# Performance work log

Hardware: AMD Instinct MI355X
Metric: run time of the kernel (lower is better)

## Reference

```python
import jax, jax.numpy as jnp
import numpy as np

NUM_HEADS = 16

def setup_inputs() -> dict:
    key = jax.random.key(0)
    ks = jax.random.split(key, 6)
    B, S, D = 2, 2048, 1024
    x = jax.random.normal(ks[0], (B, S, D), dtype=jnp.float32)
    s = 1.0 / np.sqrt(D)
    Wq = jax.random.normal(ks[1], (D, D), dtype=jnp.float32) * s
    Wk = jax.random.normal(ks[2], (D, D), dtype=jnp.float32) * s
    Wv = jax.random.normal(ks[3], (D, D), dtype=jnp.float32) * s
    Wff = jax.random.normal(ks[4], (D, D), dtype=jnp.float32) * s
    bff = jax.random.normal(ks[5], (D,), dtype=jnp.float32) * 0.01
    return {"x": x, "Wq": Wq, "Wk": Wk, "Wv": Wv, "Wff": Wff, "bff": bff}

def reference(x, Wq, Wk, Wv, Wff, bff):
    B, S, D = x.shape
    H = NUM_HEADS
    Dh = D // H
    # Q/K/V projections (bias-free Linears). Original scales Q by 1/sqrt(hidden_size).
    q = (x @ Wq.T) * (1.0 / jnp.sqrt(jnp.asarray(D, x.dtype)))
    k = x @ Wk.T
    v = x @ Wv.T
    q = q.reshape(B, S, H, Dh)
    k = k.reshape(B, S, H, Dh)
    v = v.reshape(B, S, H, Dh)
    # Blockwise online-softmax attention is mathematically identical to
    # full softmax attention over all keys (no causal mask in source).
    scores = jnp.einsum('bqhd,bkhd->bhqk', q, k)
    attn = jax.nn.softmax(scores, axis=-1)
    out = jnp.einsum('bhqk,bkhd->bqhd', attn, v).reshape(B, S, D)
    # Final feedforward Linear(hidden, hidden) with bias.
    return out @ Wff.T + bff
```

## Files before the change

kernel.cpp:

```cpp
#include <hip/hip_runtime.h>
#include <stdint.h>

typedef __attribute__((ext_vector_type(8))) short bf16x8;
typedef __attribute__((ext_vector_type(4))) float f32x4;

__device__ __forceinline__ uint16_t f2bf(float f) {
  union { float f; uint32_t u; } a; a.f = f;
  uint32_t u = a.u;
  u += 0x7FFFu + ((u >> 16) & 1u);
  return (uint16_t)(u >> 16);
}

__device__ __forceinline__ uint32_t pk_bf16(float a, float b) {
#if __has_builtin(__builtin_amdgcn_cvt_pk_bf16_f32)
  auto r = __builtin_amdgcn_cvt_pk_bf16_f32(a, b);
  uint32_t u; __builtin_memcpy(&u, &r, sizeof(u));
  return u;
#else
  return (uint32_t)f2bf(a) | ((uint32_t)f2bf(b) << 16);
#endif
}

__device__ __forceinline__ uint32_t pk_bf16_fast(float a, float b) {
#if __has_builtin(__builtin_amdgcn_cvt_pk_bf16_f32)
  auto r = __builtin_amdgcn_cvt_pk_bf16_f32(a, b);
  uint32_t u; __builtin_memcpy(&u, &r, sizeof(u));
  return u;
#else
  uint32_t ua, ub;
  __builtin_memcpy(&ua, &a, 4); __builtin_memcpy(&ub, &b, 4);
  return __builtin_amdgcn_perm(ub, ua, 0x07060302u);
#endif
}

__device__ __forceinline__ float fast_exp2(float x) {
#if __has_builtin(__builtin_amdgcn_exp2f)
  return __builtin_amdgcn_exp2f(x);
#else
  return exp2f(x);
#endif
}

__device__ __forceinline__ void gld_lds16(const uint16_t* g, uint16_t* l) {
  __builtin_amdgcn_global_load_lds(
      (const __attribute__((address_space(1))) void*)g,
      (__attribute__((address_space(3))) void*)l, 16, 0, 0);
}

__global__ void cast_all(const float* __restrict__ x, const float* __restrict__ wq,
                         const float* __restrict__ wk, const float* __restrict__ wv,
                         const float* __restrict__ wff,
                         uint16_t* __restrict__ xb, uint16_t* __restrict__ wqb,
                         uint16_t* __restrict__ wkb, uint16_t* __restrict__ wvb,
                         uint16_t* __restrict__ wffb) {
  int i = blockIdx.x * blockDim.x + threadIdx.x;
  const float* src; uint16_t* dst; int off;
  if (i < 1048576)      { src = x;   dst = xb;   off = i; }
  else if (i < 1310720) { src = wq;  dst = wqb;  off = i - 1048576; }
  else if (i < 1572864) { src = wk;  dst = wkb;  off = i - 1310720; }
  else if (i < 1835008) { src = wv;  dst = wvb;  off = i - 1572864; }
  else                  { src = wff; dst = wffb; off = i - 1835008; }
  float4 v = ((const float4*)src)[off];
  uint2 o; o.x = pk_bf16(v.x, v.y); o.y = pk_bf16(v.z, v.w);
  ((uint2*)dst)[off] = o;
}

__device__ __forceinline__ void gemm_tile(const uint16_t* __restrict__ Abase,
                                          const uint16_t* __restrict__ Bbase,
                                          uint16_t* lds, f32x4 acc[4][4]) {
  const int tid  = threadIdx.x;
  const int w    = tid >> 6;
  const int lane = tid & 63;
  const int wm   = w >> 1, wn = w & 1;
  const int lrow = lane & 15;
  const int quad = lane >> 4;
  const int srow = lane >> 3;
  const int lc   = (lane & 7) ^ srow;
  const int sx   = lrow & 7;
  uint16_t* a_lds = lds;
  uint16_t* b_lds = lds + 8192;

#pragma unroll
  for (int mt = 0; mt < 4; ++mt)
#pragma unroll
    for (int nt = 0; nt < 4; ++nt)
      acc[mt][nt] = (f32x4){0.f, 0.f, 0.f, 0.f};

  const uint16_t* ag = Abase + (size_t)(w * 32 + srow) * 1024 + lc * 8;
  const uint16_t* bg = Bbase + (size_t)(w * 32 + srow) * 1024 + lc * 8;

  for (int k0 = 0; k0 < 1024; k0 += 64) {
#pragma unroll
    for (int i8 = 0; i8 < 4; ++i8) {
      gld_lds16(ag + (size_t)i8 * 8 * 1024 + k0, a_lds + (w * 4 + i8) * 512);
      gld_lds16(bg + (size_t)i8 * 8 * 1024 + k0, b_lds + (w * 4 + i8) * 512);
    }
    __syncthreads();
#pragma unroll
    for (int ks = 0; ks < 2; ++ks) {
      bf16x8 af[4], bfr[4];
      const int c = ((ks * 4 + quad) ^ sx) << 3;
#pragma unroll
      for (int mt = 0; mt < 4; ++mt)
        af[mt] = *(const bf16x8*)(a_lds + (wm * 64 + mt * 16 + lrow) * 64 + c);
#pragma unroll
      for (int nt = 0; nt < 4; ++nt)
        bfr[nt] = *(const bf16x8*)(b_lds + (wn * 64 + nt * 16 + lrow) * 64 + c);
#pragma unroll
      for (int mt = 0; mt < 4; ++mt)
#pragma unroll
        for (int nt = 0; nt < 4; ++nt)
          acc[mt][nt] = __builtin_amdgcn_mfma_f32_16x16x32_bf16(af[mt], bfr[nt], acc[mt][nt], 0, 0, 0);
    }
    __syncthreads();
  }
}

__global__ __launch_bounds__(256) void gemm_qkv(
    const uint16_t* __restrict__ x,
    const uint16_t* __restrict__ wq, const uint16_t* __restrict__ wk, const uint16_t* __restrict__ wv,
    uint16_t* __restrict__ qo, uint16_t* __restrict__ ko, uint16_t* __restrict__ vto) {
  __shared__ __align__(16) uint16_t lds[17408];
  const int m0 = blockIdx.x * 128, n0 = blockIdx.y * 128, z = blockIdx.z;
  f32x4 acc[4][4];
  if (z < 2) {
    const uint16_t* W = (z == 0) ? wq : wk;
    gemm_tile(W + (size_t)n0 * 1024, x + (size_t)m0 * 1024, lds, acc);
  } else {
    gemm_tile(x + (size_t)m0 * 1024, wv + (size_t)n0 * 1024, lds, acc);
  }

  const int tid = threadIdx.x;
  const int lane = tid & 63, w = tid >> 6;
  const int wm = w >> 1, wn = w & 1, lrow = lane & 15, quad = lane >> 4;
  const float scale = (z == 0) ? 0.045084222f : 1.0f;

#pragma unroll
  for (int mt = 0; mt < 4; ++mt)
#pragma unroll
    for (int nt = 0; nt < 4; ++nt) {
      int i0 = wm * 64 + mt * 16 + quad * 4;
      int j  = wn * 64 + nt * 16 + lrow;
      uint2 dd;
      dd.x = pk_bf16(acc[mt][nt][0] * scale, acc[mt][nt][1] * scale);
      dd.y = pk_bf16(acc[mt][nt][2] * scale, acc[mt][nt][3] * scale);
      *(uint2*)(&lds[j * 136 + i0]) = dd;
    }
  __syncthreads();

  uint16_t* outp = (z == 0) ? qo : (z == 1) ? ko : vto;
  if (z < 2) {
#pragma unroll
    for (int it = 0; it < 8; ++it) {
      int idx = it * 256 + tid;
      int jj = idx >> 4, cc = idx & 15;
      uint4 v = *(const uint4*)(&lds[jj * 136 + cc * 8]);
      int m = m0 + jj, n = n0 + cc * 8;
      int b = m >> 11, s = m & 2047, h = n >> 6, dh = n & 63;
      *(uint4*)(outp + ((size_t)((b * 16 + h) * 2048 + s)) * 64 + dh) = v;
    }
  } else {
    int b = m0 >> 11, sbase = m0 & 2047;
#pragma unroll
    for (int it = 0; it < 8; ++it) {
      int idx = it * 256 + tid;
      int ff = idx >> 4, cc = idx & 15;
      uint4 v = *(const uint4*)(&lds[ff * 136 + cc * 8]);
      int n = n0 + ff, h = n >> 6, dh = n & 63;
      *(uint4*)(outp + ((size_t)((b * 16 + h) * 64 + dh)) * 2048 + sbase + cc * 8) = v;
    }
  }
}

__global__ __launch_bounds__(256) void gemm_ff(
    const uint16_t* __restrict__ ao, const uint16_t* __restrict__ wff,
    const float* __restrict__ bff, float* __restrict__ out) {
  __shared__ __align__(16) uint16_t lds[17408];
  const int m0 = blockIdx.x * 128, n0 = blockIdx.y * 128;
  f32x4 acc[4][4];
  gemm_tile(wff + (size_t)n0 * 1024, ao + (size_t)m0 * 1024, lds, acc);

  const int tid = threadIdx.x;
  const int lane = tid & 63, w = tid >> 6;
  const int wm = w >> 1, wn = w & 1, lrow = lane & 15, quad = lane >> 4;
  float* fl = (float*)lds;

#pragma unroll
  for (int p = 0; p < 2; ++p) {
    if (wm == p) {
#pragma unroll
      for (int mt = 0; mt < 4; ++mt)
#pragma unroll
        for (int nt = 0; nt < 4; ++nt) {
          int i0 = mt * 16 + quad * 4;
          int j  = wn * 64 + nt * 16 + lrow;
          *(f32x4*)(&fl[j * 68 + i0]) = acc[mt][nt];
        }
    }
    __syncthreads();
#pragma unroll
    for (int it = 0; it < 8; ++it) {
      int idx = it * 256 + tid;
      int jj = idx >> 4, cc = idx & 15;
      f32x4 v = *(const f32x4*)(&fl[jj * 68 + cc * 4]);
      int n = n0 + p * 64 + cc * 4;
      f32x4 bias = *(const f32x4*)(bff + n);
      f32x4 vv = v + bias;
      *(f32x4*)(out + (size_t)(m0 + jj) * 1024 + n) = vv;
    }
    __syncthreads();
  }
}

__global__ __launch_bounds__(256, 2) void attn(
    const uint16_t* __restrict__ q, const uint16_t* __restrict__ k,
    const uint16_t* __restrict__ vt, uint16_t* __restrict__ ao) {
  __shared__ __align__(16) uint16_t k_lds[2][4096];
  __shared__ __align__(16) uint16_t v_lds[2][4096];
  __shared__ __align__(16) uint16_t p_lds[2][8192];
  const int tid = threadIdx.x, w = tid >> 6, lane = tid & 63;
  const int lrow = lane & 15, quad = lane >> 4;
  const int srow = lane >> 3, lc = (lane & 7) ^ srow, sx = lrow & 7;
  const int pk = w >> 1, pq = w & 1;
  const int pswz = (lrow & 3) << 2;
  const int bh = blockIdx.y, qb = blockIdx.x;
  const uint16_t* Q = q  + (size_t)bh * (2048 * 64);
  const uint16_t* K = k  + (size_t)bh * (2048 * 64);
  const uint16_t* V = vt + (size_t)bh * (64 * 2048);

  const int qr0 = qb * 128;
  bf16x8 qf[8][2];
#pragma unroll
  for (int qh = 0; qh < 8; ++qh)
#pragma unroll
    for (int ks = 0; ks < 2; ++ks)
      qf[qh][ks] = *(const bf16x8*)(Q + (size_t)(qr0 + qh * 16 + lrow) * 64 + ks * 32 + quad * 8);

  f32x4 o[4][4];
#pragma unroll
  for (int qh = 0; qh < 4; ++qh)
#pragma unroll
    for (int dt = 0; dt < 4; ++dt) o[qh][dt] = (f32x4){0.f, 0.f, 0.f, 0.f};
  float ls[8] = {0.f, 0.f, 0.f, 0.f, 0.f, 0.f, 0.f, 0.f};
  bf16x8 vfr[4];

  auto stage = [&](int kb, int bi) {
#pragma unroll
    for (int i2 = 0; i2 < 2; ++i2) {
      int i8 = w * 2 + i2;
      gld_lds16(K + (size_t)(kb * 64 + i8 * 8 + srow) * 64 + lc * 8, &k_lds[bi][i8 * 512]);
      gld_lds16(V + (size_t)(i8 * 8 + srow) * 2048 + kb * 64 + lc * 8, &v_lds[bi][i8 * 512]);
    }
  };
  stage(0, 0);

  for (int kb = 0; kb < 32; ++kb) {
    const int bi = kb & 1;
    __syncthreads();

    if (kb > 0) {
      const uint16_t* pbuf = p_lds[bi ^ 1];
#pragma unroll
      for (int qh = 0; qh < 4; ++qh) {
        int row = pq * 64 + qh * 16 + lrow;
        bf16x8 pa = *(const bf16x8*)(pbuf + row * 64 + (((pk * 8 + quad * 2) ^ pswz) << 2));
#pragma unroll
        for (int dt = 0; dt < 4; ++dt)
          o[qh][dt] = __builtin_amdgcn_mfma_f32_16x16x32_bf16(vfr[dt], pa, o[qh][dt], 0, 0, 0);
      }
    }

#pragma unroll
    for (int dt = 0; dt < 4; ++dt)
      vfr[dt] = *(const bf16x8*)(&v_lds[bi][(dt * 16 + lrow) * 64 + (((pk * 4 + quad) ^ sx) << 3)]);

    if (kb + 1 < 32) stage(kb + 1, bi ^ 1);

    f32x4 s[8];
#pragma unroll
    for (int qh = 0; qh < 8; ++qh) s[qh] = (f32x4){0.f, 0.f, 0.f, 0.f};
#pragma unroll
    for (int ks = 0; ks < 2; ++ks) {
      bf16x8 kf = *(const bf16x8*)(&k_lds[bi][(w * 16 + lrow) * 64 + (((ks * 4 + quad) ^ sx) << 3)]);
#pragma unroll
      for (int qh = 0; qh < 8; ++qh)
        s[qh] = __builtin_amdgcn_mfma_f32_16x16x32_bf16(kf, qf[qh][ks], s[qh], 0, 0, 0);
    }

    uint16_t* pbw = p_lds[bi];
#pragma unroll
    for (int qh = 0; qh < 8; ++qh) {
      float p0 = fast_exp2(s[qh][0]);
      float p1 = fast_exp2(s[qh][1]);
      float p2 = fast_exp2(s[qh][2]);
      float p3 = fast_exp2(s[qh][3]);
      ls[qh] += (p0 + p1) + (p2 + p3);
      uint2 dd; dd.x = pk_bf16_fast(p0, p1); dd.y = pk_bf16_fast(p2, p3);
      int row = qh * 16 + lrow;
      *(uint2*)(pbw + row * 64 + (((w * 4 + quad) ^ pswz) << 2)) = dd;
    }
  }

  __syncthreads();
  {
    const uint16_t* pbuf = p_lds[1];
#pragma unroll
    for (int qh = 0; qh < 4; ++qh) {
      int row = pq * 64 + qh * 16 + lrow;
      bf16x8 pa = *(const bf16x8*)(pbuf + row * 64 + (((pk * 8 + quad * 2) ^ pswz) << 2));
#pragma unroll
      for (int dt = 0; dt < 4; ++dt)
        o[qh][dt] = __builtin_amdgcn_mfma_f32_16x16x32_bf16(vfr[dt], pa, o[qh][dt], 0, 0, 0);
    }
  }
  __syncthreads();

#pragma unroll
  for (int qh = 0; qh < 8; ++qh) {
    ls[qh] += __shfl_xor(ls[qh], 16);
    ls[qh] += __shfl_xor(ls[qh], 32);
  }
  float* lred  = (float*)&k_lds[0][0];
  float* arena = (float*)&p_lds[0][0];
  if (quad == 0) {
#pragma unroll
    for (int qh = 0; qh < 8; ++qh) lred[w * 128 + qh * 16 + lrow] = ls[qh];
  }
  if (pk == 1) {
#pragma unroll
    for (int qh = 0; qh < 4; ++qh)
#pragma unroll
      for (int dt = 0; dt < 4; ++dt)
        *(f32x4*)(&arena[(pq * 64 + qh * 16 + lrow) * 64 + dt * 16 + quad * 4]) = o[qh][dt];
  }
  __syncthreads();

  if (pk == 0) {
    const int b = bh >> 4, h = bh & 15;
#pragma unroll
    for (int qh = 0; qh < 4; ++qh) {
      int qrow = pq * 64 + qh * 16 + lrow;
      float l = lred[qrow] + lred[128 + qrow] + lred[256 + qrow] + lred[384 + qrow];
      float inv = 1.0f / l;
      int sg = qr0 + qrow;
#pragma unroll
      for (int dt = 0; dt < 4; ++dt) {
        f32x4 a = *(const f32x4*)(&arena[qrow * 64 + dt * 16 + quad * 4]);
        uint2 dd;
        dd.x = pk_bf16((o[qh][dt][0] + a[0]) * inv, (o[qh][dt][1] + a[1]) * inv);
        dd.y = pk_bf16((o[qh][dt][2] + a[2]) * inv, (o[qh][dt][3] + a[3]) * inv);
        *(uint2*)(ao + (size_t)(b * 2048 + sg) * 1024 + h * 64 + dt * 16 + quad * 4) = dd;
      }
    }
  }
}

extern "C" void kernel_launch(void* const* d_in, const int* in_sizes, int n_in,
                              void* d_out, int out_size, void* d_ws, size_t ws_size,
                              hipStream_t stream) {
  const float* x   = (const float*)d_in[0];
  const float* Wq  = (const float*)d_in[1];
  const float* Wk  = (const float*)d_in[2];
  const float* Wv  = (const float*)d_in[3];
  const float* Wff = (const float*)d_in[4];
  const float* bff = (const float*)d_in[5];
  float* out = (float*)d_out;

  uint16_t* ws = (uint16_t*)d_ws;
  uint16_t* x_bf   = ws;
  uint16_t* wq_bf  = ws + 4194304;
  uint16_t* wk_bf  = ws + 5242880;
  uint16_t* wv_bf  = ws + 6291456;
  uint16_t* wff_bf = ws + 7340032;
  uint16_t* q_bf   = ws + 8388608;
  uint16_t* k_bf   = ws + 12582912;
  uint16_t* vt_bf  = ws + 16777216;
  uint16_t* ao_bf  = ws + 20971520;

  cast_all<<<8192, 256, 0, stream>>>(x, Wq, Wk, Wv, Wff, x_bf, wq_bf, wk_bf, wv_bf, wff_bf);

  gemm_qkv<<<dim3(32, 8, 3), 256, 0, stream>>>(x_bf, wq_bf, wk_bf, wv_bf, q_bf, k_bf, vt_bf);
  attn<<<dim3(16, 32), 256, 0, stream>>>(q_bf, k_bf, vt_bf, ao_bf);
  gemm_ff<<<dim3(32, 8), 256, 0, stream>>>(ao_bf, wff_bf, bff, out);
}
```

Measured before the change: 181.3 us.

## Halve attention and FF-GEMM tile sizes to raise grid size and occupancy

Result: slower. 201.0 us (+10.9%).

```diff
diff --git a/kernel.cpp b/kernel.cpp
--- a/kernel.cpp
+++ b/kernel.cpp
@@ -175,49 +175,88 @@
 __global__ __launch_bounds__(256) void gemm_ff(
     const uint16_t* __restrict__ ao, const uint16_t* __restrict__ wff,
     const float* __restrict__ bff, float* __restrict__ out) {
-  __shared__ __align__(16) uint16_t lds[17408];
-  const int m0 = blockIdx.x * 128, n0 = blockIdx.y * 128;
-  f32x4 acc[4][4];
-  gemm_tile(wff + (size_t)n0 * 1024, ao + (size_t)m0 * 1024, lds, acc);
-
-  const int tid = threadIdx.x;
-  const int lane = tid & 63, w = tid >> 6;
-  const int wm = w >> 1, wn = w & 1, lrow = lane & 15, quad = lane >> 4;
+  __shared__ __align__(16) uint16_t lds[12288];
+  const int m0 = blockIdx.x * 128, n0 = blockIdx.y * 64;
+  const int tid  = threadIdx.x;
+  const int w    = tid >> 6;
+  const int lane = tid & 63;
+  const int wm   = w >> 1, wn = w & 1;
+  const int lrow = lane & 15;
+  const int quad = lane >> 4;
+  const int srow = lane >> 3;
+  const int lc   = (lane & 7) ^ srow;
+  const int sx   = lrow & 7;
+  uint16_t* a_lds = lds;
+  uint16_t* b_lds = lds + 4096;
+
+  f32x4 acc[4][2];
+#pragma unroll
+  for (int mt = 0; mt < 4; ++mt)
+#pragma unroll
+    for (int nt = 0; nt < 2; ++nt)
+      acc[mt][nt] = (f32x4){0.f, 0.f, 0.f, 0.f};
+
+  const uint16_t* ag = wff + (size_t)(n0 + w * 16 + srow) * 1024 + lc * 8;
+  const uint16_t* bg = ao  + (size_t)(m0 + w * 32 + srow) * 1024 + lc * 8;
+
+  for (int k0 = 0; k0 < 1024; k0 += 64) {
+#pragma unroll
+    for (int i2 = 0; i2 < 2; ++i2)
+      gld_lds16(ag + (size_t)i2 * 8 * 1024 + k0, a_lds + (w * 2 + i2) * 512);
+#pragma unroll
+    for (int i8 = 0; i8 < 4; ++i8)
+      gld_lds16(bg + (size_t)i8 * 8 * 1024 + k0, b_lds + (w * 4 + i8) * 512);
+    __syncthreads();
+#pragma unroll
+    for (int ks = 0; ks < 2; ++ks) {
+      bf16x8 af[2], bfr[4];
+      const int c = ((ks * 4 + quad) ^ sx) << 3;
+#pragma unroll
+      for (int nt = 0; nt < 2; ++nt)
+        af[nt] = *(const bf16x8*)(a_lds + (wn * 32 + nt * 16 + lrow) * 64 + c);
+#pragma unroll
+      for (int mt = 0; mt < 4; ++mt)
+        bfr[mt] = *(const bf16x8*)(b_lds + (wm * 64 + mt * 16 + lrow) * 64 + c);
+#pragma unroll
+      for (int mt = 0; mt < 4; ++mt)
+#pragma unroll
+        for (int nt = 0; nt < 2; ++nt)
+          acc[mt][nt] = __builtin_amdgcn_mfma_f32_16x16x32_bf16(af[nt], bfr[mt], acc[mt][nt], 0, 0, 0);
+    }
+    __syncthreads();
+  }
+
   float* fl = (float*)lds;
-
 #pragma unroll
   for (int p = 0; p < 2; ++p) {
     if (wm == p) {
 #pragma unroll
       for (int mt = 0; mt < 4; ++mt)
 #pragma unroll
-        for (int nt = 0; nt < 4; ++nt) {
-          int i0 = mt * 16 + quad * 4;
-          int j  = wn * 64 + nt * 16 + lrow;
-          *(f32x4*)(&fl[j * 68 + i0]) = acc[mt][nt];
-        }
-    }
-    __syncthreads();
-#pragma unroll
-    for (int it = 0; it < 8; ++it) {
+        for (int nt = 0; nt < 2; ++nt)
+          *(f32x4*)(&fl[(mt * 16 + lrow) * 68 + wn * 32 + nt * 16 + quad * 4]) = acc[mt][nt];
+    }
+    __syncthreads();
+#pragma unroll
+    for (int it = 0; it < 4; ++it) {
       int idx = it * 256 + tid;
       int jj = idx >> 4, cc = idx & 15;
       f32x4 v = *(const f32x4*)(&fl[jj * 68 + cc * 4]);
-      int n = n0 + p * 64 + cc * 4;
+      int n = n0 + cc * 4;
       f32x4 bias = *(const f32x4*)(bff + n);
       f32x4 vv = v + bias;
-      *(f32x4*)(out + (size_t)(m0 + jj) * 1024 + n) = vv;
-    }
-    __syncthreads();
-  }
-}
-
-__global__ __launch_bounds__(256, 2) void attn(
+      *(f32x4*)(out + (size_t)(m0 + p * 64 + jj) * 1024 + n) = vv;
+    }
+    __syncthreads();
+  }
+}
+
+__global__ __launch_bounds__(256, 3) void attn(
     const uint16_t* __restrict__ q, const uint16_t* __restrict__ k,
     const uint16_t* __restrict__ vt, uint16_t* __restrict__ ao) {
   __shared__ __align__(16) uint16_t k_lds[2][4096];
   __shared__ __align__(16) uint16_t v_lds[2][4096];
-  __shared__ __align__(16) uint16_t p_lds[2][8192];
+  __shared__ __align__(16) uint16_t p_lds[2][4096];
   const int tid = threadIdx.x, w = tid >> 6, lane = tid & 63;
   const int lrow = lane & 15, quad = lane >> 4;
   const int srow = lane >> 3, lc = (lane & 7) ^ srow, sx = lrow & 7;
@@ -228,20 +267,20 @@
   const uint16_t* K = k  + (size_t)bh * (2048 * 64);
   const uint16_t* V = vt + (size_t)bh * (64 * 2048);
 
-  const int qr0 = qb * 128;
-  bf16x8 qf[8][2];
-#pragma unroll
-  for (int qh = 0; qh < 8; ++qh)
+  const int qr0 = qb * 64;
+  bf16x8 qf[4][2];
+#pragma unroll
+  for (int qh = 0; qh < 4; ++qh)
 #pragma unroll
     for (int ks = 0; ks < 2; ++ks)
       qf[qh][ks] = *(const bf16x8*)(Q + (size_t)(qr0 + qh * 16 + lrow) * 64 + ks * 32 + quad * 8);
 
-  f32x4 o[4][4];
-#pragma unroll
-  for (int qh = 0; qh < 4; ++qh)
+  f32x4 o[2][4];
+#pragma unroll
+  for (int qh = 0; qh < 2; ++qh)
 #pragma unroll
     for (int dt = 0; dt < 4; ++dt) o[qh][dt] = (f32x4){0.f, 0.f, 0.f, 0.f};
-  float ls[8] = {0.f, 0.f, 0.f, 0.f, 0.f, 0.f, 0.f, 0.f};
+  float ls[4] = {0.f, 0.f, 0.f, 0.f};
   bf16x8 vfr[4];
 
   auto stage = [&](int kb, int bi) {
@@ -260,14 +299,16 @@
 
     if (kb > 0) {
       const uint16_t* pbuf = p_lds[bi ^ 1];
-#pragma unroll
-      for (int qh = 0; qh < 4; ++qh) {
-        int row = pq * 64 + qh * 16 + lrow;
+      __builtin_amdgcn_s_setprio(1);
+#pragma unroll
+      for (int qh = 0; qh < 2; ++qh) {
+        int row = pq * 32 + qh * 16 + lrow;
         bf16x8 pa = *(const bf16x8*)(pbuf + row * 64 + (((pk * 8 + quad * 2) ^ pswz) << 2));
 #pragma unroll
         for (int dt = 0; dt < 4; ++dt)
           o[qh][dt] = __builtin_amdgcn_mfma_f32_16x16x32_bf16(vfr[dt], pa, o[qh][dt], 0, 0, 0);
       }
+      __builtin_amdgcn_s_setprio(0);
     }
 
 #pragma unroll
@@ -276,20 +317,22 @@
 
     if (kb + 1 < 32) stage(kb + 1, bi ^ 1);
 
-    f32x4 s[8];
-#pragma unroll
-    for (int qh = 0; qh < 8; ++qh) s[qh] = (f32x4){0.f, 0.f, 0.f, 0.f};
+    f32x4 s[4];
+#pragma unroll
+    for (int qh = 0; qh < 4; ++qh) s[qh] = (f32x4){0.f, 0.f, 0.f, 0.f};
+    __builtin_amdgcn_s_setprio(1);
 #pragma unroll
     for (int ks = 0; ks < 2; ++ks) {
       bf16x8 kf = *(const bf16x8*)(&k_lds[bi][(w * 16 + lrow) * 64 + (((ks * 4 + quad) ^ sx) << 3)]);
 #pragma unroll
-      for (int qh = 0; qh < 8; ++qh)
+      for (int qh = 0; qh < 4; ++qh)
         s[qh] = __builtin_amdgcn_mfma_f32_16x16x32_bf16(kf, qf[qh][ks], s[qh], 0, 0, 0);
     }
+    __builtin_amdgcn_s_setprio(0);
 
     uint16_t* pbw = p_lds[bi];
 #pragma unroll
-    for (int qh = 0; qh < 8; ++qh) {
+    for (int qh = 0; qh < 4; ++qh) {
       float p0 = fast_exp2(s[qh][0]);
       float p1 = fast_exp2(s[qh][1]);
       float p2 = fast_exp2(s[qh][2]);
@@ -305,8 +348,8 @@
   {
     const uint16_t* pbuf = p_lds[1];
 #pragma unroll
-    for (int qh = 0; qh < 4; ++qh) {
-      int row = pq * 64 + qh * 16 + lrow;
+    for (int qh = 0; qh < 2; ++qh) {
+      int row = pq * 32 + qh * 16 + lrow;
       bf16x8 pa = *(const bf16x8*)(pbuf + row * 64 + (((pk * 8 + quad * 2) ^ pswz) << 2));
 #pragma unroll
       for (int dt = 0; dt < 4; ++dt)
@@ -316,7 +359,7 @@
   __syncthreads();
 
 #pragma unroll
-  for (int qh = 0; qh < 8; ++qh) {
+  for (int qh = 0; qh < 4; ++qh) {
     ls[qh] += __shfl_xor(ls[qh], 16);
     ls[qh] += __shfl_xor(ls[qh], 32);
   }
@@ -324,23 +367,23 @@
   float* arena = (float*)&p_lds[0][0];
   if (quad == 0) {
 #pragma unroll
-    for (int qh = 0; qh < 8; ++qh) lred[w * 128 + qh * 16 + lrow] = ls[qh];
+    for (int qh = 0; qh < 4; ++qh) lred[w * 64 + qh * 16 + lrow] = ls[qh];
   }
   if (pk == 1) {
 #pragma unroll
-    for (int qh = 0; qh < 4; ++qh)
+    for (int qh = 0; qh < 2; ++qh)
 #pragma unroll
       for (int dt = 0; dt < 4; ++dt)
-        *(f32x4*)(&arena[(pq * 64 + qh * 16 + lrow) * 64 + dt * 16 + quad * 4]) = o[qh][dt];
+        *(f32x4*)(&arena[(pq * 32 + qh * 16 + lrow) * 64 + dt * 16 + quad * 4]) = o[qh][dt];
   }
   __syncthreads();
 
   if (pk == 0) {
     const int b = bh >> 4, h = bh & 15;
 #pragma unroll
-    for (int qh = 0; qh < 4; ++qh) {
-      int qrow = pq * 64 + qh * 16 + lrow;
-      float l = lred[qrow] + lred[128 + qrow] + lred[256 + qrow] + lred[384 + qrow];
+    for (int qh = 0; qh < 2; ++qh) {
+      int qrow = pq * 32 + qh * 16 + lrow;
+      float l = lred[qrow] + lred[64 + qrow] + lred[128 + qrow] + lred[192 + qrow];
       float inv = 1.0f / l;
       int sg = qr0 + qrow;
 #pragma unroll
@@ -380,6 +423,6 @@
   cast_all<<<8192, 256, 0, stream>>>(x, Wq, Wk, Wv, Wff, x_bf, wq_bf, wk_bf, wv_bf, wff_bf);
 
   gemm_qkv<<<dim3(32, 8, 3), 256, 0, stream>>>(x_bf, wq_bf, wk_bf, wv_bf, q_bf, k_bf, vt_bf);
-  attn<<<dim3(16, 32), 256, 0, stream>>>(q_bf, k_bf, vt_bf, ao_bf);
-  gemm_ff<<<dim3(32, 8), 256, 0, stream>>>(ao_bf, wff_bf, bff, out);
-}
+  attn<<<dim3(32, 32), 256, 0, stream>>>(q_bf, k_bf, vt_bf, ao_bf);
+  gemm_ff<<<dim3(32, 16), 256, 0, stream>>>(ao_bf, wff_bf, bff, out);
+}
```

## Single-buffer P tile to fit three attention blocks per CU, add MFMA priority

Applied to the files above, without the earlier changes.

New measurement: 279.9 us. +54.3%, slower.

```diff
diff --git a/kernel.cpp b/kernel.cpp
--- a/kernel.cpp
+++ b/kernel.cpp
@@ -212,12 +212,13 @@
   }
 }
 
-__global__ __launch_bounds__(256, 2) void attn(
+__global__ __launch_bounds__(256, 3) void attn(
     const uint16_t* __restrict__ q, const uint16_t* __restrict__ k,
     const uint16_t* __restrict__ vt, uint16_t* __restrict__ ao) {
-  __shared__ __align__(16) uint16_t k_lds[2][4096];
-  __shared__ __align__(16) uint16_t v_lds[2][4096];
-  __shared__ __align__(16) uint16_t p_lds[2][8192];
+  __shared__ __align__(16) uint16_t lds_all[24576];
+  uint16_t* const k_lds = lds_all;
+  uint16_t* const v_lds = lds_all + 8192;
+  uint16_t* const p_lds = lds_all + 16384;
   const int tid = threadIdx.x, w = tid >> 6, lane = tid & 63;
   const int lrow = lane & 15, quad = lane >> 4;
   const int srow = lane >> 3, lc = (lane & 7) ^ srow, sx = lrow & 7;
@@ -248,8 +249,8 @@
 #pragma unroll
     for (int i2 = 0; i2 < 2; ++i2) {
       int i8 = w * 2 + i2;
-      gld_lds16(K + (size_t)(kb * 64 + i8 * 8 + srow) * 64 + lc * 8, &k_lds[bi][i8 * 512]);
-      gld_lds16(V + (size_t)(i8 * 8 + srow) * 2048 + kb * 64 + lc * 8, &v_lds[bi][i8 * 512]);
+      gld_lds16(K + (size_t)(kb * 64 + i8 * 8 + srow) * 64 + lc * 8, k_lds + bi * 4096 + i8 * 512);
+      gld_lds16(V + (size_t)(i8 * 8 + srow) * 2048 + kb * 64 + lc * 8, v_lds + bi * 4096 + i8 * 512);
     }
   };
   stage(0, 0);
@@ -258,36 +259,40 @@
     const int bi = kb & 1;
     __syncthreads();
 
+    if (kb + 1 < 32) stage(kb + 1, bi ^ 1);
+
     if (kb > 0) {
-      const uint16_t* pbuf = p_lds[bi ^ 1];
+      __builtin_amdgcn_s_setprio(1);
 #pragma unroll
       for (int qh = 0; qh < 4; ++qh) {
         int row = pq * 64 + qh * 16 + lrow;
-        bf16x8 pa = *(const bf16x8*)(pbuf + row * 64 + (((pk * 8 + quad * 2) ^ pswz) << 2));
+        bf16x8 pa = *(const bf16x8*)(p_lds + row * 64 + (((pk * 8 + quad * 2) ^ pswz) << 2));
 #pragma unroll
         for (int dt = 0; dt < 4; ++dt)
           o[qh][dt] = __builtin_amdgcn_mfma_f32_16x16x32_bf16(vfr[dt], pa, o[qh][dt], 0, 0, 0);
       }
+      __builtin_amdgcn_s_setprio(0);
     }
 
 #pragma unroll
     for (int dt = 0; dt < 4; ++dt)
-      vfr[dt] = *(const bf16x8*)(&v_lds[bi][(dt * 16 + lrow) * 64 + (((pk * 4 + quad) ^ sx) << 3)]);
-
-    if (kb + 1 < 32) stage(kb + 1, bi ^ 1);
+      vfr[dt] = *(const bf16x8*)(v_lds + bi * 4096 + (dt * 16 + lrow) * 64 + (((pk * 4 + quad) ^ sx) << 3));
 
     f32x4 s[8];
 #pragma unroll
     for (int qh = 0; qh < 8; ++qh) s[qh] = (f32x4){0.f, 0.f, 0.f, 0.f};
+    __builtin_amdgcn_s_setprio(1);
 #pragma unroll
     for (int ks = 0; ks < 2; ++ks) {
-      bf16x8 kf = *(const bf16x8*)(&k_lds[bi][(w * 16 + lrow) * 64 + (((ks * 4 + quad) ^ sx) << 3)]);
+      bf16x8 kf = *(const bf16x8*)(k_lds + bi * 4096 + (w * 16 + lrow) * 64 + (((ks * 4 + quad) ^ sx) << 3));
 #pragma unroll
       for (int qh = 0; qh < 8; ++qh)
         s[qh] = __builtin_amdgcn_mfma_f32_16x16x32_bf16(kf, qf[qh][ks], s[qh], 0, 0, 0);
     }
-
-    uint16_t* pbw = p_lds[bi];
+    __builtin_amdgcn_s_setprio(0);
+
+    __syncthreads();
+
 #pragma unroll
     for (int qh = 0; qh < 8; ++qh) {
       float p0 = fast_exp2(s[qh][0]);
@@ -297,21 +302,22 @@
       ls[qh] += (p0 + p1) + (p2 + p3);
       uint2 dd; dd.x = pk_bf16_fast(p0, p1); dd.y = pk_bf16_fast(p2, p3);
       int row = qh * 16 + lrow;
-      *(uint2*)(pbw + row * 64 + (((w * 4 + quad) ^ pswz) << 2)) = dd;
+      *(uint2*)(p_lds + row * 64 + (((w * 4 + quad) ^ pswz) << 2)) = dd;
     }
   }
 
   __syncthreads();
   {
-    const uint16_t* pbuf = p_lds[1];
+    __builtin_amdgcn_s_setprio(1);
 #pragma unroll
     for (int qh = 0; qh < 4; ++qh) {
       int row = pq * 64 + qh * 16 + lrow;
-      bf16x8 pa = *(const bf16x8*)(pbuf + row * 64 + (((pk * 8 + quad * 2) ^ pswz) << 2));
+      bf16x8 pa = *(const bf16x8*)(p_lds + row * 64 + (((pk * 8 + quad * 2) ^ pswz) << 2));
 #pragma unroll
       for (int dt = 0; dt < 4; ++dt)
         o[qh][dt] = __builtin_amdgcn_mfma_f32_16x16x32_bf16(vfr[dt], pa, o[qh][dt], 0, 0, 0);
     }
+    __builtin_amdgcn_s_setprio(0);
   }
   __syncthreads();
 
@@ -320,8 +326,8 @@
     ls[qh] += __shfl_xor(ls[qh], 16);
     ls[qh] += __shfl_xor(ls[qh], 32);
   }
-  float* lred  = (float*)&k_lds[0][0];
-  float* arena = (float*)&p_lds[0][0];
+  float* lred  = (float*)(lds_all + 16384);
+  float* arena = (float*)lds_all;
   if (quad == 0) {
 #pragma unroll
     for (int qh = 0; qh < 8; ++qh) lred[w * 128 + qh * 16 + lrow] = ls[qh];
```
